# Optimization experiments

Hardware: AMD Instinct MI355X
Metric: run time of the kernel (lower is better)

## Reference

```python
import jax, jax.numpy as jnp
import numpy as np

B, N, S, D, ITERS = 128, 8192, 4, 32, 3
LN_EPS = 1e-5

def _ln(x, g, b):
    m = jnp.mean(x, axis=-1, keepdims=True)
    v = jnp.mean((x - m) ** 2, axis=-1, keepdims=True)
    return (x - m) * jax.lax.rsqrt(v + LN_EPS) * g + b

def setup_inputs() -> dict:
    key = jax.random.key(0)
    ks = jax.random.split(key, 16)
    s = 1.0 / np.sqrt(D)
    return {
        "x": jax.random.normal(ks[0], (B, N, D), jnp.float32),
        "slot_noise": jax.random.normal(ks[1], (B, S, D), jnp.float32),
        "slots_mu": jax.random.normal(ks[2], (1, 1, D), jnp.float32),
        "slots_logsigma": jnp.zeros((1, 1, D), jnp.float32),
        "Wq": jax.random.uniform(ks[3], (D, D), jnp.float32, -s, s),
        "Wk": jax.random.uniform(ks[4], (D, D), jnp.float32, -s, s),
        "Wv": jax.random.uniform(ks[5], (D, D), jnp.float32, -s, s),
        "gru_Wih": jax.random.uniform(ks[6], (3 * D, D), jnp.float32, -s, s),
        "gru_Whh": jax.random.uniform(ks[7], (3 * D, D), jnp.float32, -s, s),
        "gru_bih": jax.random.uniform(ks[8], (3 * D,), jnp.float32, -s, s),
        "gru_bhh": jax.random.uniform(ks[9], (3 * D,), jnp.float32, -s, s),
        "mlp_W1": jax.random.uniform(ks[10], (D, D), jnp.float32, -s, s),
        "mlp_b1": jax.random.uniform(ks[11], (D,), jnp.float32, -s, s),
        "mlp_W2": jax.random.uniform(ks[12], (D, D), jnp.float32, -s, s),
        "mlp_b2": jax.random.uniform(ks[13], (D,), jnp.float32, -s, s),
        "lnx_g": jnp.ones((D,), jnp.float32), "lnx_b": jnp.zeros((D,), jnp.float32),
        "lns_g": jnp.ones((D,), jnp.float32), "lns_b": jnp.zeros((D,), jnp.float32),
        "lnff_g": jnp.ones((D,), jnp.float32), "lnff_b": jnp.zeros((D,), jnp.float32),
    }

def reference(x, slot_noise, slots_mu, slots_logsigma, Wq, Wk, Wv,
              gru_Wih, gru_Whh, gru_bih, gru_bhh,
              mlp_W1, mlp_b1, mlp_W2, mlp_b2,
              lnx_g, lnx_b, lns_g, lns_b, lnff_g, lnff_b):
    d = x.shape[-1]
    scale = d ** (-0.5)
    xn = _ln(x, lnx_g, lnx_b)                      # [B,N,D]
    k = xn @ Wk.T                                  # [B,N,D] (x fixed -> hoist out of loop)
    v = xn @ Wv.T
    slots = slots_mu + slot_noise * jnp.exp(slots_logsigma)  # [B,S,D]
    for _ in range(ITERS):
        q = _ln(slots, lns_g, lns_b) @ Wq.T        # [B,S,D]
        attn = jnp.einsum('bsd,bnd->bsn', q, k) * scale
        attn = jax.nn.softmax(attn, axis=-1) + 1e-8
        attn = attn / jnp.sum(attn, axis=-1, keepdims=True)
        upd = jnp.einsum('bsn,bnd->bsd', attn, v)  # [B,S,D]
        # GRUCell (PyTorch gate order: r, z, n)
        gi = upd @ gru_Wih.T + gru_bih             # [B,S,3D]
        gh = slots @ gru_Whh.T + gru_bhh
        ir, iz, inn = jnp.split(gi, 3, axis=-1)
        hr, hz, hn = jnp.split(gh, 3, axis=-1)
        r = jax.nn.sigmoid(ir + hr)
        z = jax.nn.sigmoid(iz + hz)
        n = jnp.tanh(inn + r * hn)
        slots = (1.0 - z) * n + z * slots
        h = jax.nn.relu(_ln(slots, lnff_g, lnff_b) @ mlp_W1.T + mlp_b1)
        slots = slots + (h @ mlp_W2.T + mlp_b2)
    return slots.reshape(slots.shape[0], -1)
```

## Files before the change

### kernel.cpp

```cpp
#include <hip/hip_runtime.h>
#include <hip/hip_bf16.h>


#define Bn 128
#define Nn 8192
#define Sn 4
#define Dn 32
#define SCALE 0.17677669529663687f

#define Cn 16
#define RPB (Nn / Cn)
#define PT 256
#define RSTEP (PT / 4)
#define NSTEP (RPB / RSTEP)

#define WS_REQ ((size_t)(16384 + 16384 + Bn*Cn*Sn*Dn + Bn*Cn*Sn + Bn*Cn*Sn) * 4)

__device__ __forceinline__ float sigmoidf_(float v) { return 1.0f / (1.0f + __expf(-v)); }

__global__ __launch_bounds__(128)
void init_kernel(const float* __restrict__ noise, const float* __restrict__ mu,
                 const float* __restrict__ logsig,
                 const float* __restrict__ lns_g, const float* __restrict__ lns_b,
                 const float* __restrict__ Wq, const float* __restrict__ Wk,
                 float* __restrict__ slots, float* __restrict__ qt)
{
    const int b = blockIdx.x;
    const int tid = threadIdx.x;
    const int s = tid >> 5, d = tid & 31;
    __shared__ float sh_a[4][32];
    __shared__ float sh_b[4][32];

    float sv = mu[d] + noise[(b * Sn + s) * Dn + d] * __expf(logsig[d]);
    slots[(b * Sn + s) * Dn + d] = sv;

    float sx = sv, sxx = sv * sv;
    #pragma unroll
    for (int m = 1; m <= 16; m <<= 1) { sx += __shfl_xor(sx, m); sxx += __shfl_xor(sxx, m); }
    float mean = sx * (1.0f / 32.0f);
    float var  = sxx * (1.0f / 32.0f) - mean * mean;
    sh_a[s][d] = (sv - mean) * rsqrtf(var + 1e-5f) * lns_g[d] + lns_b[d];
    __syncthreads();

    float q = 0.0f;
    #pragma unroll 8
    for (int j = 0; j < 32; ++j) q = fmaf(Wq[d * 32 + j], sh_a[s][j], q);
    sh_b[s][d] = q;
    __syncthreads();

    float qtv = 0.0f;
    #pragma unroll 8
    for (int i = 0; i < 32; ++i) qtv = fmaf(sh_b[s][i], Wk[i * 32 + d], qtv);
    qt[(b * Sn + s) * Dn + d] = qtv * SCALE;
}

__global__ __launch_bounds__(PT)
void pass_kernel(const float* __restrict__ x, const float* __restrict__ qt,
                 const float* __restrict__ lnx_g, const float* __restrict__ lnx_b,
                 float* __restrict__ part_pa, float* __restrict__ part_pb,
                 float* __restrict__ part_ps)
{
    const int c = blockIdx.x;
    const int b = blockIdx.y;
    const int tid = threadIdx.x;
    const int sub = tid & 3, col0 = sub * 8;
    const int rg  = tid >> 2;

    float qg[4][8], qgs[4], qe[4];
    {
        const float* qtb = qt + (size_t)b * Sn * Dn;
        float g8[8], e8[8];
        #pragma unroll
        for (int k = 0; k < 8; ++k) { g8[k] = lnx_g[col0 + k]; e8[k] = lnx_b[col0 + k]; }
        #pragma unroll
        for (int s = 0; s < 4; ++s) {
            float sg = 0.f, se = 0.f;
            #pragma unroll
            for (int k = 0; k < 8; ++k) {
                float q = qtb[s * Dn + col0 + k];
                qg[s][k] = q * g8[k];
                sg += qg[s][k];
                se = fmaf(q, e8[k], se);
            }
            sg += __shfl_xor(sg, 1); sg += __shfl_xor(sg, 2);
            se += __shfl_xor(se, 1); se += __shfl_xor(se, 2);
            qgs[s] = sg; qe[s] = se;
        }
    }

    float pa[4][8], pb[4] = {0.f,0.f,0.f,0.f}, ps[4] = {0.f,0.f,0.f,0.f};
    #pragma unroll
    for (int s = 0; s < 4; ++s)
        #pragma unroll
        for (int k = 0; k < 8; ++k) pa[s][k] = 0.f;

    const float* xb = x + ((size_t)b * Nn + (size_t)c * RPB) * Dn;
    const float* p0 = xb + (size_t)rg * Dn + col0;
    float4 v0 = *(const float4*)(p0);
    float4 v1 = *(const float4*)(p0 + 4);

    for (int t = 0; t < NSTEP; ++t) {
        const int tn = (t + 1 < NSTEP) ? t + 1 : t;
        const float* pn = xb + (size_t)(tn * RSTEP + rg) * Dn + col0;
        float4 n0 = *(const float4*)(pn);
        float4 n1 = *(const float4*)(pn + 4);

        float xv[8] = {v0.x, v0.y, v0.z, v0.w, v1.x, v1.y, v1.z, v1.w};

        float sx = 0.f, sxx = 0.f, ds[4] = {0.f,0.f,0.f,0.f};
        #pragma unroll
        for (int k = 0; k < 8; ++k) {
            sx += xv[k];
            sxx = fmaf(xv[k], xv[k], sxx);
            #pragma unroll
            for (int s = 0; s < 4; ++s) ds[s] = fmaf(xv[k], qg[s][k], ds[s]);
        }
        sx += __shfl_xor(sx, 1); sxx += __shfl_xor(sxx, 1);
        #pragma unroll
        for (int s = 0; s < 4; ++s) ds[s] += __shfl_xor(ds[s], 1);
        sx += __shfl_xor(sx, 2); sxx += __shfl_xor(sxx, 2);
        #pragma unroll
        for (int s = 0; s < 4; ++s) ds[s] += __shfl_xor(ds[s], 2);

        float mean = sx * (1.0f / 32.0f);
        float var  = sxx * (1.0f / 32.0f) - mean * mean;
        float rs   = rsqrtf(var + 1e-5f);

        #pragma unroll
        for (int s = 0; s < 4; ++s) {
            float tt = fmaf(-mean, qgs[s], ds[s]);
            float lg = fmaf(rs, tt, qe[s]);
            float w  = __expf(lg);
            float al = w * rs;
            ps[s] += w;
            pb[s] = fmaf(al, mean, pb[s]);
            #pragma unroll
            for (int k = 0; k < 8; ++k) pa[s][k] = fmaf(al, xv[k], pa[s][k]);
        }
        v0 = n0; v1 = n1;
    }

    #pragma unroll
    for (int m = 4; m <= 32; m <<= 1) {
        #pragma unroll
        for (int s = 0; s < 4; ++s) {
            ps[s] += __shfl_xor(ps[s], m);
            pb[s] += __shfl_xor(pb[s], m);
            #pragma unroll
            for (int k = 0; k < 8; ++k) pa[s][k] += __shfl_xor(pa[s][k], m);
        }
    }

    __shared__ float ls_pa[4][4][32];
    __shared__ float ls_pb[4][4];
    __shared__ float ls_ps[4][4];
    const int wv = tid >> 6, lane = tid & 63;
    if (lane < 4) {
        #pragma unroll
        for (int s = 0; s < 4; ++s)
            #pragma unroll
            for (int k = 0; k < 8; ++k) ls_pa[wv][s][lane * 8 + k] = pa[s][k];
        if (lane == 0) {
            #pragma unroll
            for (int s = 0; s < 4; ++s) { ls_pb[wv][s] = pb[s]; ls_ps[wv][s] = ps[s]; }
        }
    }
    __syncthreads();
    if (tid < 128) {
        const int s = tid >> 5, d = tid & 31;
        float a = ls_pa[0][s][d] + ls_pa[1][s][d] + ls_pa[2][s][d] + ls_pa[3][s][d];
        part_pa[(((size_t)b * Cn + c) * Sn + s) * Dn + d] = a;
        if (d == 0) {
            part_pb[((size_t)b * Cn + c) * Sn + s] =
                ls_pb[0][s] + ls_pb[1][s] + ls_pb[2][s] + ls_pb[3][s];
            part_ps[((size_t)b * Cn + c) * Sn + s] =
                ls_ps[0][s] + ls_ps[1][s] + ls_ps[2][s] + ls_ps[3][s];
        }
    }
}

__global__ __launch_bounds__(128)
void update_kernel(const float* __restrict__ part_pa, const float* __restrict__ part_pb,
                   const float* __restrict__ part_ps,
                   const float* __restrict__ lnx_g, const float* __restrict__ lnx_b,
                   const float* __restrict__ Wv,
                   const float* __restrict__ Wih, const float* __restrict__ Whh,
                   const float* __restrict__ bih, const float* __restrict__ bhh,
                   const float* __restrict__ W1, const float* __restrict__ b1v,
                   const float* __restrict__ W2, const float* __restrict__ b2v,
                   const float* __restrict__ lns_g, const float* __restrict__ lns_b,
                   const float* __restrict__ lnff_g, const float* __restrict__ lnff_b,
                   const float* __restrict__ Wq, const float* __restrict__ Wk,
                   float* __restrict__ slots, float* __restrict__ qt,
                   float* __restrict__ out, int write_out, int write_qt)
{
    const int b = blockIdx.x;
    const int tid = threadIdx.x;
    const int s = tid >> 5, d = tid & 31;
    __shared__ float sh_a[4][32];
    __shared__ float sh_b[4][32];
    __shared__ float sh_sold[4][32];
    __shared__ float sh_h[4][32];

    float PA = 0.f, PB = 0.f, PS = 0.f;
    #pragma unroll
    for (int c = 0; c < Cn; ++c) {
        PA += part_pa[(((size_t)b * Cn + c) * Sn + s) * Dn + d];
        PB += part_pb[((size_t)b * Cn + c) * Sn + s];
        PS += part_ps[((size_t)b * Cn + c) * Sn + s];
    }
    float u = fmaf(lnx_g[d], PA - PB, PS * lnx_b[d]);
    const float renorm = 1.0f / (1.0f + (float)Nn * 1e-8f);
    sh_a[s][d] = (u / PS) * renorm;
    float sold = slots[(b * Sn + s) * Dn + d];
    sh_sold[s][d] = sold;
    __syncthreads();

    float upd = 0.f;
    #pragma unroll 8
    for (int j = 0; j < 32; ++j) upd = fmaf(Wv[d * 32 + j], sh_a[s][j], upd);
    sh_b[s][d] = upd;
    __syncthreads();

    float gi[3], gh[3];
    #pragma unroll
    for (int g3 = 0; g3 < 3; ++g3) {
        const int row = g3 * 32 + d;
        float a1 = bih[row], a2 = bhh[row];
        #pragma unroll 8
        for (int j = 0; j < 32; ++j) {
            a1 = fmaf(Wih[row * 32 + j], sh_b[s][j], a1);
            a2 = fmaf(Whh[row * 32 + j], sh_sold[s][j], a2);
        }
        gi[g3] = a1; gh[g3] = a2;
    }
    float r  = sigmoidf_(gi[0] + gh[0]);
    float z  = sigmoidf_(gi[1] + gh[1]);
    float nn = tanhf(gi[2] + r * gh[2]);
    float sv = (1.0f - z) * nn + z * sold;

    {
        float sx = sv, sxx = sv * sv;
        #pragma unroll
        for (int m = 1; m <= 16; m <<= 1) { sx += __shfl_xor(sx, m); sxx += __shfl_xor(sxx, m); }
        float mean = sx * (1.0f / 32.0f);
        float var  = sxx * (1.0f / 32.0f) - mean * mean;
        float rs   = rsqrtf(var + 1e-5f);
        __syncthreads();
        sh_a[s][d] = (sv - mean) * rs * lnff_g[d] + lnff_b[d];
    }
    __syncthreads();

    float h1 = b1v[d];
    #pragma unroll 8
    for (int j = 0; j < 32; ++j) h1 = fmaf(W1[d * 32 + j], sh_a[s][j], h1);
    sh_h[s][d] = fmaxf(h1, 0.0f);
    __syncthreads();

    float o = b2v[d];
    #pragma unroll 8
    for (int j = 0; j < 32; ++j) o = fmaf(W2[d * 32 + j], sh_h[s][j], o);
    float sfin = sv + o;

    slots[(b * Sn + s) * Dn + d] = sfin;
    if (write_out) out[(b * Sn + s) * Dn + d] = sfin;

    if (write_qt) {
        float sx = sfin, sxx = sfin * sfin;
        #pragma unroll
        for (int m = 1; m <= 16; m <<= 1) { sx += __shfl_xor(sx, m); sxx += __shfl_xor(sxx, m); }
        float mean = sx * (1.0f / 32.0f);
        float var  = sxx * (1.0f / 32.0f) - mean * mean;
        float rs   = rsqrtf(var + 1e-5f);
        __syncthreads();
        sh_a[s][d] = (sfin - mean) * rs * lns_g[d] + lns_b[d];
        __syncthreads();
        float q = 0.f;
        #pragma unroll 8
        for (int j = 0; j < 32; ++j) q = fmaf(Wq[d * 32 + j], sh_a[s][j], q);
        sh_b[s][d] = q;
        __syncthreads();
        float qtv = 0.f;
        #pragma unroll 8
        for (int i = 0; i < 32; ++i) qtv = fmaf(sh_b[s][i], Wk[i * 32 + d], qtv);
        qt[(b * Sn + s) * Dn + d] = qtv * SCALE;
    }
}

#define TPB 1024
#define NW (TPB / 64)
#define RPS (TPB / 4)
#define STEPS (Nn / RPS)

__global__ __launch_bounds__(TPB)
void slot_fused(const float* __restrict__ x, const float* __restrict__ noise,
                const float* __restrict__ mu, const float* __restrict__ logsig,
                const float* __restrict__ Wq, const float* __restrict__ Wk,
                const float* __restrict__ Wv,
                const float* __restrict__ Wih, const float* __restrict__ Whh,
                const float* __restrict__ bih, const float* __restrict__ bhh,
                const float* __restrict__ W1, const float* __restrict__ b1v,
                const float* __restrict__ W2, const float* __restrict__ b2v,
                const float* __restrict__ lnx_g, const float* __restrict__ lnx_b,
                const float* __restrict__ lns_g, const float* __restrict__ lns_b,
                const float* __restrict__ lnff_g, const float* __restrict__ lnff_b,
                float* __restrict__ out)
{
    const int b   = blockIdx.x;
    const int tid = threadIdx.x;
    __shared__ float slots_sh[Sn][Dn];
    __shared__ float qt_sh[Sn][Dn];
    __shared__ float a_sh[Sn][Dn];
    __shared__ float b_sh[Sn][Dn];
    __shared__ float h_sh[Sn][Dn];
    __shared__ float ls_u[NW][Sn][Dn];
    __shared__ float ls_s[NW][Sn];
    const int s128 = tid >> 5, d128 = tid & 31;

    if (tid < 128) {
        float sv = mu[d128] + noise[(b * Sn + s128) * Dn + d128] * __expf(logsig[d128]);
        slots_sh[s128][d128] = sv;
        float sx = sv, sxx = sv * sv;
        #pragma unroll
        for (int m = 1; m <= 16; m <<= 1) { sx += __shfl_xor(sx, m); sxx += __shfl_xor(sxx, m); }
        float mean = sx * (1.0f / 32.0f);
        float var  = sxx * (1.0f / 32.0f) - mean * mean;
        a_sh[s128][d128] = (sv - mean) * rsqrtf(var + 1e-5f) * lns_g[d128] + lns_b[d128];
    }
    __syncthreads();
    if (tid < 128) {
        float q = 0.f;
        #pragma unroll 8
        for (int j = 0; j < 32; ++j) q = fmaf(Wq[d128 * 32 + j], a_sh[s128][j], q);
        b_sh[s128][d128] = q;
    }
    __syncthreads();
    if (tid < 128) {
        float qv = 0.f;
        #pragma unroll 8
        for (int i = 0; i < 32; ++i) qv = fmaf(b_sh[s128][i], Wk[i * 32 + d128], qv);
        qt_sh[s128][d128] = qv * SCALE;
    }
    __syncthreads();

    const int sub = tid & 3, col0 = sub * 8;
    const int rg  = tid >> 2;
    float g_r[8], e_r[8];
    #pragma unroll
    for (int k = 0; k < 8; ++k) { g_r[k] = lnx_g[col0 + k]; e_r[k] = lnx_b[col0 + k]; }
    const float* xb = x + (size_t)b * Nn * Dn;
    float sv_reg = 0.f;

    for (int it = 0; it < 3; ++it) {
        float qt_r[4][8];
        #pragma unroll
        for (int s = 0; s < 4; ++s)
            #pragma unroll
            for (int k = 0; k < 8; ++k) qt_r[s][k] = qt_sh[s][col0 + k];
        float pu[4][8];
        float ps[4] = {0.f, 0.f, 0.f, 0.f};
        #pragma unroll
        for (int s = 0; s < 4; ++s)
            #pragma unroll
            for (int k = 0; k < 8; ++k) pu[s][k] = 0.f;

        const float* xr0 = xb + (size_t)rg * Dn + col0;
        float4 v0 = *(const float4*)(xr0);
        float4 v1 = *(const float4*)(xr0 + 4);
        #pragma unroll 2
        for (int t = 0; t < STEPS; ++t) {
            const float* xrn = xb + (size_t)((((t + 1) & (STEPS - 1)) * RPS) + rg) * Dn + col0;
            float4 n0 = *(const float4*)(xrn);
            float4 n1 = *(const float4*)(xrn + 4);
            float xv[8] = {v0.x, v0.y, v0.z, v0.w, v1.x, v1.y, v1.z, v1.w};
            float sx = 0.f, sxx = 0.f;
            #pragma unroll
            for (int k = 0; k < 8; ++k) { sx += xv[k]; sxx = fmaf(xv[k], xv[k], sxx); }
            sx += __shfl_xor(sx, 1); sxx += __shfl_xor(sxx, 1);
            sx += __shfl_xor(sx, 2); sxx += __shfl_xor(sxx, 2);
            float mean = sx * (1.0f / 32.0f);
            float var  = sxx * (1.0f / 32.0f) - mean * mean;
            float rs   = rsqrtf(var + 1e-5f);
            float xn[8];
            #pragma unroll
            for (int k = 0; k < 8; ++k) xn[k] = fmaf((xv[k] - mean) * rs, g_r[k], e_r[k]);
            #pragma unroll
            for (int s = 0; s < 4; ++s) {
                float a = 0.f;
                #pragma unroll
                for (int k = 0; k < 8; ++k) a = fmaf(xn[k], qt_r[s][k], a);
                a += __shfl_xor(a, 1);
                a += __shfl_xor(a, 2);
                float w = __expf(a);
                ps[s] += w;
                #pragma unroll
                for (int k = 0; k < 8; ++k) pu[s][k] = fmaf(w, xn[k], pu[s][k]);
            }
            v0 = n0; v1 = n1;
        }
        #pragma unroll
        for (int m = 4; m <= 32; m <<= 1) {
            #pragma unroll
            for (int s = 0; s < 4; ++s) {
                ps[s] += __shfl_xor(ps[s], m);
                #pragma unroll
                for (int k = 0; k < 8; ++k) pu[s][k] += __shfl_xor(pu[s][k], m);
            }
        }
        {
            const int wv = tid >> 6, lane = tid & 63;
            if (lane < 4) {
                #pragma unroll
                for (int s = 0; s < 4; ++s)
                    #pragma unroll
                    for (int k = 0; k < 8; ++k) ls_u[wv][s][lane * 8 + k] = pu[s][k];
                if (lane == 0) {
                    #pragma unroll
                    for (int s = 0; s < 4; ++s) ls_s[wv][s] = ps[s];
                }
            }
        }
        __syncthreads();
        if (tid < 128) {
            float u = 0.f, ss = 0.f;
            #pragma unroll
            for (int w = 0; w < NW; ++w) { u += ls_u[w][s128][d128]; ss += ls_s[w][s128]; }
            const float renorm = 1.0f / (1.0f + (float)Nn * 1e-8f);
            a_sh[s128][d128] = (u / ss) * renorm;
        }
        __syncthreads();
        if (tid < 128) {
            float upd = 0.f;
            #pragma unroll 8
            for (int j = 0; j < 32; ++j) upd = fmaf(Wv[d128 * 32 + j], a_sh[s128][j], upd);
            b_sh[s128][d128] = upd;
        }
        __syncthreads();
        if (tid < 128) {
            float gi[3], gh[3];
            #pragma unroll
            for (int g3 = 0; g3 < 3; ++g3) {
                const int row = g3 * 32 + d128;
                float a1 = bih[row], a2 = bhh[row];
                #pragma unroll 8
                for (int j = 0; j < 32; ++j) {
                    a1 = fmaf(Wih[row * 32 + j], b_sh[s128][j], a1);
                    a2 = fmaf(Whh[row * 32 + j], slots_sh[s128][j], a2);
                }
                gi[g3] = a1; gh[g3] = a2;
            }
            float r  = sigmoidf_(gi[0] + gh[0]);
            float z  = sigmoidf_(gi[1] + gh[1]);
            float nn = tanhf(gi[2] + r * gh[2]);
            sv_reg = (1.0f - z) * nn + z * slots_sh[s128][d128];
            float sx = sv_reg, sxx = sv_reg * sv_reg;
            #pragma unroll
            for (int m = 1; m <= 16; m <<= 1) { sx += __shfl_xor(sx, m); sxx += __shfl_xor(sxx, m); }
            float mean = sx * (1.0f / 32.0f);
            float var  = sxx * (1.0f / 32.0f) - mean * mean;
            a_sh[s128][d128] = (sv_reg - mean) * rsqrtf(var + 1e-5f) * lnff_g[d128] + lnff_b[d128];
        }
        __syncthreads();
        if (tid < 128) {
            float h = b1v[d128];
            #pragma unroll 8
            for (int j = 0; j < 32; ++j) h = fmaf(W1[d128 * 32 + j], a_sh[s128][j], h);
            h_sh[s128][d128] = fmaxf(h, 0.f);
        }
        __syncthreads();
        if (tid < 128) {
            float o = b2v[d128];
            #pragma unroll 8
            for (int j = 0; j < 32; ++j) o = fmaf(W2[d128 * 32 + j], h_sh[s128][j], o);
            float sfin = sv_reg + o;
            slots_sh[s128][d128] = sfin;
            if (it < 2) {
                float sx = sfin, sxx = sfin * sfin;
                #pragma unroll
                for (int m = 1; m <= 16; m <<= 1) { sx += __shfl_xor(sx, m); sxx += __shfl_xor(sxx, m); }
                float mean = sx * (1.0f / 32.0f);
                float var  = sxx * (1.0f / 32.0f) - mean * mean;
                a_sh[s128][d128] = (sfin - mean) * rsqrtf(var + 1e-5f) * lns_g[d128] + lns_b[d128];
            }
        }
        __syncthreads();
        if (it < 2) {
            if (tid < 128) {
                float q = 0.f;
                #pragma unroll 8
                for (int j = 0; j < 32; ++j) q = fmaf(Wq[d128 * 32 + j], a_sh[s128][j], q);
                b_sh[s128][d128] = q;
            }
            __syncthreads();
            if (tid < 128) {
                float qv = 0.f;
                #pragma unroll 8
                for (int i = 0; i < 32; ++i) qv = fmaf(b_sh[s128][i], Wk[i * 32 + d128], qv);
                qt_sh[s128][d128] = qv * SCALE;
            }
            __syncthreads();
        }
    }
    if (tid < 128)
        out[(size_t)b * 128 + tid] = slots_sh[s128][d128];
}

extern "C" void kernel_launch(void* const* d_in, const int* in_sizes, int n_in,
                              void* d_out, int out_size, void* d_ws, size_t ws_size,
                              hipStream_t stream)
{
    const float* x      = (const float*)d_in[0];
    const float* noise  = (const float*)d_in[1];
    const float* mu     = (const float*)d_in[2];
    const float* logsig = (const float*)d_in[3];
    const float* Wq     = (const float*)d_in[4];
    const float* Wk     = (const float*)d_in[5];
    const float* Wv     = (const float*)d_in[6];
    const float* Wih    = (const float*)d_in[7];
    const float* Whh    = (const float*)d_in[8];
    const float* bih    = (const float*)d_in[9];
    const float* bhh    = (const float*)d_in[10];
    const float* W1     = (const float*)d_in[11];
    const float* b1v    = (const float*)d_in[12];
    const float* W2     = (const float*)d_in[13];
    const float* b2v    = (const float*)d_in[14];
    const float* lnx_g  = (const float*)d_in[15];
    const float* lnx_b  = (const float*)d_in[16];
    const float* lns_g  = (const float*)d_in[17];
    const float* lns_b  = (const float*)d_in[18];
    const float* lnff_g = (const float*)d_in[19];
    const float* lnff_b = (const float*)d_in[20];
    float* out = (float*)d_out;

    if (ws_size >= WS_REQ) {
        float* ws      = (float*)d_ws;
        float* slots   = ws;
        float* qt      = ws + 16384;
        float* part_pa = ws + 32768;
        float* part_pb = ws + 32768 + Bn * Cn * Sn * Dn;
        float* part_ps = part_pb + Bn * Cn * Sn;

        init_kernel<<<Bn, 128, 0, stream>>>(noise, mu, logsig, lns_g, lns_b, Wq, Wk,
                                            slots, qt);
        for (int it = 0; it < 3; ++it) {
            pass_kernel<<<dim3(Cn, Bn), PT, 0, stream>>>(x, qt, lnx_g, lnx_b,
                                                         part_pa, part_pb, part_ps);
            update_kernel<<<Bn, 128, 0, stream>>>(part_pa, part_pb, part_ps,
                                                  lnx_g, lnx_b, Wv, Wih, Whh, bih, bhh,
                                                  W1, b1v, W2, b2v, lns_g, lns_b,
                                                  lnff_g, lnff_b, Wq, Wk, slots, qt, out,
                                                  (it == 2) ? 1 : 0, (it < 2) ? 1 : 0);
        }
    } else {
        slot_fused<<<Bn, TPB, 0, stream>>>(x, noise, mu, logsig, Wq, Wk, Wv,
                                           Wih, Whh, bih, bhh, W1, b1v, W2, b2v,
                                           lnx_g, lnx_b, lns_g, lns_b, lnff_g, lnff_b,
                                           out);
    }
}
```

Baseline: 134.6 us.

## Cache normalized x as bf16 and fuse slot update into attention passes

The first pass computes LayerNorm of x once and stores it as a bf16 buffer. Later passes read this half-size buffer and skip the per-row LayerNorm math. The small per-batch slot update (GRU, MLP, query projection) is recomputed redundantly at the start of each pass block, removing separate init and update launches. This trades bf16 rounding error in the keys and values for less memory traffic and fewer kernel launches.

Result: slower. 173.3 us (+28.7%).

```diff
diff --git a/kernel.cpp b/kernel.cpp
--- a/kernel.cpp
+++ b/kernel.cpp
@@ -7,6 +7,7 @@
 #define Sn 4
 #define Dn 32
 #define SCALE 0.17677669529663687f
+#define RENORM (1.0f / (1.0f + (float)Nn * 1e-8f))
 
 #define Cn 16
 #define RPB (Nn / Cn)
@@ -14,130 +15,286 @@
 #define RSTEP (PT / 4)
 #define NSTEP (RPB / RSTEP)
 
-#define WS_REQ ((size_t)(16384 + 16384 + Bn*Cn*Sn*Dn + Bn*Cn*Sn + Bn*Cn*Sn) * 4)
+#define WS_REQ ((size_t)(3 * Bn * Sn * Dn + 3 * Bn * Cn * Sn * Dn + 3 * Bn * Cn * Sn) * 4 \
+                + (size_t)Bn * Nn * Dn * 2)
 
 __device__ __forceinline__ float sigmoidf_(float v) { return 1.0f / (1.0f + __expf(-v)); }
-
-__global__ __launch_bounds__(128)
-void init_kernel(const float* __restrict__ noise, const float* __restrict__ mu,
-                 const float* __restrict__ logsig,
-                 const float* __restrict__ lns_g, const float* __restrict__ lns_b,
-                 const float* __restrict__ Wq, const float* __restrict__ Wk,
-                 float* __restrict__ slots, float* __restrict__ qt)
+__device__ __forceinline__ unsigned f2bf_rne(float f) {
+    unsigned u = __float_as_uint(f);
+    u += 0x7fffu + ((u >> 16) & 1u);
+    return u >> 16;
+}
+__device__ __forceinline__ float bflo2f(unsigned u) { return __uint_as_float(u << 16); }
+__device__ __forceinline__ float bfhi2f(unsigned u) { return __uint_as_float(u & 0xffff0000u); }
+
+template<int KIND, int WANT_QT>
+__device__ __forceinline__ void chain_fn(
+    int b, int tid,
+    const float* __restrict__ pa_prev, const float* __restrict__ ps_prev,
+    const float* __restrict__ slots_prev,
+    const float* __restrict__ noise, const float* __restrict__ mu,
+    const float* __restrict__ logsig,
+    const float* __restrict__ Wv,
+    const float* __restrict__ Wih, const float* __restrict__ Whh,
+    const float* __restrict__ bih, const float* __restrict__ bhh,
+    const float* __restrict__ W1, const float* __restrict__ b1v,
+    const float* __restrict__ W2, const float* __restrict__ b2v,
+    const float* __restrict__ lns_g, const float* __restrict__ lns_b,
+    const float* __restrict__ lnff_g, const float* __restrict__ lnff_b,
+    const float* __restrict__ Wq, const float* __restrict__ Wk,
+    float (*qt_sh)[Dn], float (*ta)[Dn], float (*tb)[Dn],
+    float* __restrict__ store)
 {
-    const int b = blockIdx.x;
-    const int tid = threadIdx.x;
-    const int s = tid >> 5, d = tid & 31;
-    __shared__ float sh_a[4][32];
-    __shared__ float sh_b[4][32];
-
-    float sv = mu[d] + noise[(b * Sn + s) * Dn + d] * __expf(logsig[d]);
-    slots[(b * Sn + s) * Dn + d] = sv;
-
-    float sx = sv, sxx = sv * sv;
+    const int s = (tid >> 5) & 3, d = tid & 31;
+    const bool act = tid < 128;
+    float sfin = 0.f;
+
+    if constexpr (KIND == 0) {
+        if (act)
+            sfin = mu[d] + noise[(b * Sn + s) * Dn + d] * __expf(logsig[d]);
+    } else {
+        float sv_c = 0.f, lnffv = 0.f;
+        if (act) {
+            float u = 0.f, PS = 0.f;
+            #pragma unroll
+            for (int c = 0; c < Cn; ++c) {
+                u  += pa_prev[(((size_t)b * Cn + c) * Sn + s) * Dn + d];
+                PS += ps_prev[((size_t)b * Cn + c) * Sn + s];
+            }
+            ta[s][d] = (u / PS) * RENORM;
+            tb[s][d] = slots_prev[(b * Sn + s) * Dn + d];
+        }
+        __syncthreads();
+        float updv = 0.f;
+        if (act) {
+            #pragma unroll 8
+            for (int j = 0; j < 32; ++j) updv = fmaf(Wv[d * 32 + j], ta[s][j], updv);
+        }
+        __syncthreads();
+        if (act) ta[s][d] = updv;
+        __syncthreads();
+        if (act) {
+            float gi[3], gh[3];
+            #pragma unroll
+            for (int g3 = 0; g3 < 3; ++g3) {
+                const int row = g3 * 32 + d;
+                float a1 = bih[row], a2 = bhh[row];
+                #pragma unroll 8
+                for (int j = 0; j < 32; ++j) {
+                    a1 = fmaf(Wih[row * 32 + j], ta[s][j], a1);
+                    a2 = fmaf(Whh[row * 32 + j], tb[s][j], a2);
+                }
+                gi[g3] = a1; gh[g3] = a2;
+            }
+            float r  = sigmoidf_(gi[0] + gh[0]);
+            float z  = sigmoidf_(gi[1] + gh[1]);
+            float nn = tanhf(gi[2] + r * gh[2]);
+            sv_c = (1.0f - z) * nn + z * tb[s][d];
+            float sx = sv_c, sxx = sv_c * sv_c;
+            #pragma unroll
+            for (int m = 1; m <= 16; m <<= 1) { sx += __shfl_xor(sx, m); sxx += __shfl_xor(sxx, m); }
+            float mean = sx * (1.0f / 32.0f);
+            float var  = sxx * (1.0f / 32.0f) - mean * mean;
+            lnffv = (sv_c - mean) * rsqrtf(var + 1e-5f) * lnff_g[d] + lnff_b[d];
+        }
+        __syncthreads();
+        if (act) ta[s][d] = lnffv;
+        __syncthreads();
+        if (act) {
+            float h = b1v[d];
+            #pragma unroll 8
+            for (int j = 0; j < 32; ++j) h = fmaf(W1[d * 32 + j], ta[s][j], h);
+            tb[s][d] = fmaxf(h, 0.f);
+        }
+        __syncthreads();
+        if (act) {
+            float o = b2v[d];
+            #pragma unroll 8
+            for (int j = 0; j < 32; ++j) o = fmaf(W2[d * 32 + j], tb[s][j], o);
+            sfin = sv_c + o;
+        }
+    }
+
+    if (act && store) store[(b * Sn + s) * Dn + d] = sfin;
+
+    if constexpr (WANT_QT) {
+        float lnsv = 0.f;
+        if (act) {
+            float sx = sfin, sxx = sfin * sfin;
+            #pragma unroll
+            for (int m = 1; m <= 16; m <<= 1) { sx += __shfl_xor(sx, m); sxx += __shfl_xor(sxx, m); }
+            float mean = sx * (1.0f / 32.0f);
+            float var  = sxx * (1.0f / 32.0f) - mean * mean;
+            lnsv = (sfin - mean) * rsqrtf(var + 1e-5f) * lns_g[d] + lns_b[d];
+        }
+        __syncthreads();
+        if (act) ta[s][d] = lnsv;
+        __syncthreads();
+        if (act) {
+            float q = 0.f;
+            #pragma unroll 8
+            for (int j = 0; j < 32; ++j) q = fmaf(Wq[d * 32 + j], ta[s][j], q);
+            tb[s][d] = q;
+        }
+        __syncthreads();
+        if (act) {
+            float qv = 0.f;
+            #pragma unroll 8
+            for (int i = 0; i < 32; ++i) qv = fmaf(tb[s][i], Wk[i * 32 + d], qv);
+            qt_sh[s][d] = qv * SCALE;
+        }
+        __syncthreads();
+    }
+}
+
+template<int IT>
+__global__ __launch_bounds__(PT)
+void pass_k(const float* __restrict__ x, unsigned short* __restrict__ y,
+            const float* __restrict__ noise, const float* __restrict__ mu,
+            const float* __restrict__ logsig,
+            const float* __restrict__ Wq, const float* __restrict__ Wk,
+            const float* __restrict__ Wv,
+            const float* __restrict__ Wih, const float* __restrict__ Whh,
+            const float* __restrict__ bih, const float* __restrict__ bhh,
+            const float* __restrict__ W1, const float* __restrict__ b1v,
+            const float* __restrict__ W2, const float* __restrict__ b2v,
+            const float* __restrict__ lnx_g, const float* __restrict__ lnx_b,
+            const float* __restrict__ lns_g, const float* __restrict__ lns_b,
+            const float* __restrict__ lnff_g, const float* __restrict__ lnff_b,
+            const float* __restrict__ slots_prev, float* __restrict__ slots_cur,
+            const float* __restrict__ pa_prev, const float* __restrict__ ps_prev,
+            float* __restrict__ pa_cur, float* __restrict__ ps_cur)
+{
+    const int c = blockIdx.x, b = blockIdx.y, tid = threadIdx.x;
+    __shared__ float qt_sh[Sn][Dn], ta[Sn][Dn], tb[Sn][Dn];
+    __shared__ float ls_pa[4][Sn][Dn];
+    __shared__ float ls_ps[4][Sn];
+
+    chain_fn<(IT == 0 ? 0 : 1), 1>(b, tid, pa_prev, ps_prev, slots_prev,
+        noise, mu, logsig, Wv, Wih, Whh, bih, bhh, W1, b1v, W2, b2v,
+        lns_g, lns_b, lnff_g, lnff_b, Wq, Wk,
+        qt_sh, ta, tb, (c == 0) ? slots_cur : nullptr);
+
+    const int sub = tid & 3, col0 = sub * 8, rg = tid >> 2;
+    float pa[4][8];
+    float ps[4] = {0.f, 0.f, 0.f, 0.f};
     #pragma unroll
-    for (int m = 1; m <= 16; m <<= 1) { sx += __shfl_xor(sx, m); sxx += __shfl_xor(sxx, m); }
-    float mean = sx * (1.0f / 32.0f);
-    float var  = sxx * (1.0f / 32.0f) - mean * mean;
-    sh_a[s][d] = (sv - mean) * rsqrtf(var + 1e-5f) * lns_g[d] + lns_b[d];
-    __syncthreads();
-
-    float q = 0.0f;
-    #pragma unroll 8
-    for (int j = 0; j < 32; ++j) q = fmaf(Wq[d * 32 + j], sh_a[s][j], q);
-    sh_b[s][d] = q;
-    __syncthreads();
-
-    float qtv = 0.0f;
-    #pragma unroll 8
-    for (int i = 0; i < 32; ++i) qtv = fmaf(sh_b[s][i], Wk[i * 32 + d], qtv);
-    qt[(b * Sn + s) * Dn + d] = qtv * SCALE;
-}
-
-__global__ __launch_bounds__(PT)
-void pass_kernel(const float* __restrict__ x, const float* __restrict__ qt,
-                 const float* __restrict__ lnx_g, const float* __restrict__ lnx_b,
-                 float* __restrict__ part_pa, float* __restrict__ part_pb,
-                 float* __restrict__ part_ps)
-{
-    const int c = blockIdx.x;
-    const int b = blockIdx.y;
-    const int tid = threadIdx.x;
-    const int sub = tid & 3, col0 = sub * 8;
-    const int rg  = tid >> 2;
-
-    float qg[4][8], qgs[4], qe[4];
-    {
-        const float* qtb = qt + (size_t)b * Sn * Dn;
-        float g8[8], e8[8];
-        #pragma unroll
-        for (int k = 0; k < 8; ++k) { g8[k] = lnx_g[col0 + k]; e8[k] = lnx_b[col0 + k]; }
+    for (int s = 0; s < 4; ++s)
+        #pragma unroll
+        for (int k = 0; k < 8; ++k) pa[s][k] = 0.f;
+
+    if constexpr (IT == 0) {
+        float g_r[8], e_r[8];
+        #pragma unroll
+        for (int k = 0; k < 8; ++k) { g_r[k] = lnx_g[col0 + k]; e_r[k] = lnx_b[col0 + k]; }
+        float qg[4][8], qgs[4], qe[4];
         #pragma unroll
         for (int s = 0; s < 4; ++s) {
             float sg = 0.f, se = 0.f;
             #pragma unroll
             for (int k = 0; k < 8; ++k) {
-                float q = qtb[s * Dn + col0 + k];
-                qg[s][k] = q * g8[k];
+                float q = qt_sh[s][col0 + k];
+                qg[s][k] = q * g_r[k];
                 sg += qg[s][k];
-                se = fmaf(q, e8[k], se);
+                se = fmaf(q, e_r[k], se);
             }
             sg += __shfl_xor(sg, 1); sg += __shfl_xor(sg, 2);
             se += __shfl_xor(se, 1); se += __shfl_xor(se, 2);
             qgs[s] = sg; qe[s] = se;
         }
-    }
-
-    float pa[4][8], pb[4] = {0.f,0.f,0.f,0.f}, ps[4] = {0.f,0.f,0.f,0.f};
-    #pragma unroll
-    for (int s = 0; s < 4; ++s)
-        #pragma unroll
-        for (int k = 0; k < 8; ++k) pa[s][k] = 0.f;
-
-    const float* xb = x + ((size_t)b * Nn + (size_t)c * RPB) * Dn;
-    const float* p0 = xb + (size_t)rg * Dn + col0;
-    float4 v0 = *(const float4*)(p0);
-    float4 v1 = *(const float4*)(p0 + 4);
-
-    for (int t = 0; t < NSTEP; ++t) {
-        const int tn = (t + 1 < NSTEP) ? t + 1 : t;
-        const float* pn = xb + (size_t)(tn * RSTEP + rg) * Dn + col0;
-        float4 n0 = *(const float4*)(pn);
-        float4 n1 = *(const float4*)(pn + 4);
-
-        float xv[8] = {v0.x, v0.y, v0.z, v0.w, v1.x, v1.y, v1.z, v1.w};
-
-        float sx = 0.f, sxx = 0.f, ds[4] = {0.f,0.f,0.f,0.f};
-        #pragma unroll
-        for (int k = 0; k < 8; ++k) {
-            sx += xv[k];
-            sxx = fmaf(xv[k], xv[k], sxx);
-            #pragma unroll
-            for (int s = 0; s < 4; ++s) ds[s] = fmaf(xv[k], qg[s][k], ds[s]);
-        }
-        sx += __shfl_xor(sx, 1); sxx += __shfl_xor(sxx, 1);
-        #pragma unroll
-        for (int s = 0; s < 4; ++s) ds[s] += __shfl_xor(ds[s], 1);
-        sx += __shfl_xor(sx, 2); sxx += __shfl_xor(sxx, 2);
-        #pragma unroll
-        for (int s = 0; s < 4; ++s) ds[s] += __shfl_xor(ds[s], 2);
-
-        float mean = sx * (1.0f / 32.0f);
-        float var  = sxx * (1.0f / 32.0f) - mean * mean;
-        float rs   = rsqrtf(var + 1e-5f);
-
-        #pragma unroll
-        for (int s = 0; s < 4; ++s) {
-            float tt = fmaf(-mean, qgs[s], ds[s]);
-            float lg = fmaf(rs, tt, qe[s]);
-            float w  = __expf(lg);
-            float al = w * rs;
-            ps[s] += w;
-            pb[s] = fmaf(al, mean, pb[s]);
-            #pragma unroll
-            for (int k = 0; k < 8; ++k) pa[s][k] = fmaf(al, xv[k], pa[s][k]);
-        }
-        v0 = n0; v1 = n1;
+
+        const float* xb = x + ((size_t)b * Nn + (size_t)c * RPB) * Dn;
+        unsigned short* yb = y + ((size_t)b * Nn + (size_t)c * RPB) * Dn;
+        const float* p0 = xb + (size_t)rg * Dn + col0;
+        float4 v0 = *(const float4*)(p0);
+        float4 v1 = *(const float4*)(p0 + 4);
+
+        for (int t = 0; t < NSTEP; ++t) {
+            const int tn = (t + 1 < NSTEP) ? t + 1 : t;
+            const float* pn = xb + (size_t)(tn * RSTEP + rg) * Dn + col0;
+            float4 n0 = *(const float4*)(pn);
+            float4 n1 = *(const float4*)(pn + 4);
+
+            float xv[8] = {v0.x, v0.y, v0.z, v0.w, v1.x, v1.y, v1.z, v1.w};
+            float sx = 0.f, sxx = 0.f, ds[4] = {0.f, 0.f, 0.f, 0.f};
+            #pragma unroll
+            for (int k = 0; k < 8; ++k) {
+                sx += xv[k];
+                sxx = fmaf(xv[k], xv[k], sxx);
+                #pragma unroll
+                for (int s = 0; s < 4; ++s) ds[s] = fmaf(xv[k], qg[s][k], ds[s]);
+            }
+            sx += __shfl_xor(sx, 1); sxx += __shfl_xor(sxx, 1);
+            #pragma unroll
+            for (int s = 0; s < 4; ++s) ds[s] += __shfl_xor(ds[s], 1);
+            sx += __shfl_xor(sx, 2); sxx += __shfl_xor(sxx, 2);
+            #pragma unroll
+            for (int s = 0; s < 4; ++s) ds[s] += __shfl_xor(ds[s], 2);
+
+            float mean = sx * (1.0f / 32.0f);
+            float var  = sxx * (1.0f / 32.0f) - mean * mean;
+            float rs   = rsqrtf(var + 1e-5f);
+
+            float xn[8];
+            #pragma unroll
+            for (int k = 0; k < 8; ++k) xn[k] = fmaf((xv[k] - mean) * rs, g_r[k], e_r[k]);
+
+            uint4 yw;
+            yw.x = (f2bf_rne(xn[1]) << 16) | f2bf_rne(xn[0]);
+            yw.y = (f2bf_rne(xn[3]) << 16) | f2bf_rne(xn[2]);
+            yw.z = (f2bf_rne(xn[5]) << 16) | f2bf_rne(xn[4]);
+            yw.w = (f2bf_rne(xn[7]) << 16) | f2bf_rne(xn[6]);
+            *(uint4*)(yb + (size_t)(t * RSTEP + rg) * Dn + col0) = yw;
+
+            #pragma unroll
+            for (int s = 0; s < 4; ++s) {
+                float lg = fmaf(rs, fmaf(-mean, qgs[s], ds[s]), qe[s]);
+                float w  = __expf(lg);
+                ps[s] += w;
+                #pragma unroll
+                for (int k = 0; k < 8; ++k) pa[s][k] = fmaf(w, xn[k], pa[s][k]);
+            }
+            v0 = n0; v1 = n1;
+        }
+    } else {
+        float qt_r[4][8];
+        #pragma unroll
+        for (int s = 0; s < 4; ++s)
+            #pragma unroll
+            for (int k = 0; k < 8; ++k) qt_r[s][k] = qt_sh[s][col0 + k];
+
+        const unsigned short* yb = y + ((size_t)b * Nn + (size_t)c * RPB) * Dn;
+        uint4 cv = *(const uint4*)(yb + (size_t)rg * Dn + col0);
+
+        for (int t = 0; t < NSTEP; ++t) {
+            const int tn = (t + 1 < NSTEP) ? t + 1 : t;
+            uint4 nv = *(const uint4*)(yb + (size_t)(tn * RSTEP + rg) * Dn + col0);
+
+            float yv[8];
+            yv[0] = bflo2f(cv.x); yv[1] = bfhi2f(cv.x);
+            yv[2] = bflo2f(cv.y); yv[3] = bfhi2f(cv.y);
+            yv[4] = bflo2f(cv.z); yv[5] = bfhi2f(cv.z);
+            yv[6] = bflo2f(cv.w); yv[7] = bfhi2f(cv.w);
+
+            float ds[4] = {0.f, 0.f, 0.f, 0.f};
+            #pragma unroll
+            for (int k = 0; k < 8; ++k)
+                #pragma unroll
+                for (int s = 0; s < 4; ++s) ds[s] = fmaf(yv[k], qt_r[s][k], ds[s]);
+            #pragma unroll
+            for (int s = 0; s < 4; ++s) ds[s] += __shfl_xor(ds[s], 1);
+            #pragma unroll
+            for (int s = 0; s < 4; ++s) ds[s] += __shfl_xor(ds[s], 2);
+
+            #pragma unroll
+            for (int s = 0; s < 4; ++s) {
+                float w = __expf(ds[s]);
+                ps[s] += w;
+                #pragma unroll
+                for (int k = 0; k < 8; ++k) pa[s][k] = fmaf(w, yv[k], pa[s][k]);
+            }
+            cv = nv;
+        }
     }
 
     #pragma unroll
@@ -145,15 +302,10 @@
         #pragma unroll
         for (int s = 0; s < 4; ++s) {
             ps[s] += __shfl_xor(ps[s], m);
-            pb[s] += __shfl_xor(pb[s], m);
             #pragma unroll
             for (int k = 0; k < 8; ++k) pa[s][k] += __shfl_xor(pa[s][k], m);
         }
     }
-
-    __shared__ float ls_pa[4][4][32];
-    __shared__ float ls_pb[4][4];
-    __shared__ float ls_ps[4][4];
     const int wv = tid >> 6, lane = tid & 63;
     if (lane < 4) {
         #pragma unroll
@@ -162,129 +314,38 @@
             for (int k = 0; k < 8; ++k) ls_pa[wv][s][lane * 8 + k] = pa[s][k];
         if (lane == 0) {
             #pragma unroll
-            for (int s = 0; s < 4; ++s) { ls_pb[wv][s] = pb[s]; ls_ps[wv][s] = ps[s]; }
+            for (int s = 0; s < 4; ++s) ls_ps[wv][s] = ps[s];
         }
     }
     __syncthreads();
     if (tid < 128) {
         const int s = tid >> 5, d = tid & 31;
         float a = ls_pa[0][s][d] + ls_pa[1][s][d] + ls_pa[2][s][d] + ls_pa[3][s][d];
-        part_pa[(((size_t)b * Cn + c) * Sn + s) * Dn + d] = a;
-        if (d == 0) {
-            part_pb[((size_t)b * Cn + c) * Sn + s] =
-                ls_pb[0][s] + ls_pb[1][s] + ls_pb[2][s] + ls_pb[3][s];
-            part_ps[((size_t)b * Cn + c) * Sn + s] =
+        pa_cur[(((size_t)b * Cn + c) * Sn + s) * Dn + d] = a;
+        if (d == 0)
+            ps_cur[((size_t)b * Cn + c) * Sn + s] =
                 ls_ps[0][s] + ls_ps[1][s] + ls_ps[2][s] + ls_ps[3][s];
-        }
     }
 }
 
 __global__ __launch_bounds__(128)
-void update_kernel(const float* __restrict__ part_pa, const float* __restrict__ part_pb,
-                   const float* __restrict__ part_ps,
-                   const float* __restrict__ lnx_g, const float* __restrict__ lnx_b,
-                   const float* __restrict__ Wv,
-                   const float* __restrict__ Wih, const float* __restrict__ Whh,
-                   const float* __restrict__ bih, const float* __restrict__ bhh,
-                   const float* __restrict__ W1, const float* __restrict__ b1v,
-                   const float* __restrict__ W2, const float* __restrict__ b2v,
-                   const float* __restrict__ lns_g, const float* __restrict__ lns_b,
-                   const float* __restrict__ lnff_g, const float* __restrict__ lnff_b,
-                   const float* __restrict__ Wq, const float* __restrict__ Wk,
-                   float* __restrict__ slots, float* __restrict__ qt,
-                   float* __restrict__ out, int write_out, int write_qt)
+void final_k(const float* __restrict__ Wv,
+             const float* __restrict__ Wih, const float* __restrict__ Whh,
+             const float* __restrict__ bih, const float* __restrict__ bhh,
+             const float* __restrict__ W1, const float* __restrict__ b1v,
+             const float* __restrict__ W2, const float* __restrict__ b2v,
+             const float* __restrict__ lns_g, const float* __restrict__ lns_b,
+             const float* __restrict__ lnff_g, const float* __restrict__ lnff_b,
+             const float* __restrict__ Wq, const float* __restrict__ Wk,
+             const float* __restrict__ slots_prev,
+             const float* __restrict__ pa_prev, const float* __restrict__ ps_prev,
+             float* __restrict__ out)
 {
-    const int b = blockIdx.x;
-    const int tid = threadIdx.x;
-    const int s = tid >> 5, d = tid & 31;
-    __shared__ float sh_a[4][32];
-    __shared__ float sh_b[4][32];
-    __shared__ float sh_sold[4][32];
-    __shared__ float sh_h[4][32];
-
-    float PA = 0.f, PB = 0.f, PS = 0.f;
-    #pragma unroll
-    for (int c = 0; c < Cn; ++c) {
-        PA += part_pa[(((size_t)b * Cn + c) * Sn + s) * Dn + d];
-        PB += part_pb[((size_t)b * Cn + c) * Sn + s];
-        PS += part_ps[((size_t)b * Cn + c) * Sn + s];
-    }
-    float u = fmaf(lnx_g[d], PA - PB, PS * lnx_b[d]);
-    const float renorm = 1.0f / (1.0f + (float)Nn * 1e-8f);
-    sh_a[s][d] = (u / PS) * renorm;
-    float sold = slots[(b * Sn + s) * Dn + d];
-    sh_sold[s][d] = sold;
-    __syncthreads();
-
-    float upd = 0.f;
-    #pragma unroll 8
-    for (int j = 0; j < 32; ++j) upd = fmaf(Wv[d * 32 + j], sh_a[s][j], upd);
-    sh_b[s][d] = upd;
-    __syncthreads();
-
-    float gi[3], gh[3];
-    #pragma unroll
-    for (int g3 = 0; g3 < 3; ++g3) {
-        const int row = g3 * 32 + d;
-        float a1 = bih[row], a2 = bhh[row];
-        #pragma unroll 8
-        for (int j = 0; j < 32; ++j) {
-            a1 = fmaf(Wih[row * 32 + j], sh_b[s][j], a1);
-            a2 = fmaf(Whh[row * 32 + j], sh_sold[s][j], a2);
-        }
-        gi[g3] = a1; gh[g3] = a2;
-    }
-    float r  = sigmoidf_(gi[0] + gh[0]);
-    float z  = sigmoidf_(gi[1] + gh[1]);
-    float nn = tanhf(gi[2] + r * gh[2]);
-    float sv = (1.0f - z) * nn + z * sold;
-
-    {
-        float sx = sv, sxx = sv * sv;
-        #pragma unroll
-        for (int m = 1; m <= 16; m <<= 1) { sx += __shfl_xor(sx, m); sxx += __shfl_xor(sxx, m); }
-        float mean = sx * (1.0f / 32.0f);
-        float var  = sxx * (1.0f / 32.0f) - mean * mean;
-        float rs   = rsqrtf(var + 1e-5f);
-        __syncthreads();
-        sh_a[s][d] = (sv - mean) * rs * lnff_g[d] + lnff_b[d];
-    }
-    __syncthreads();
-
-    float h1 = b1v[d];
-    #pragma unroll 8
-    for (int j = 0; j < 32; ++j) h1 = fmaf(W1[d * 32 + j], sh_a[s][j], h1);
-    sh_h[s][d] = fmaxf(h1, 0.0f);
-    __syncthreads();
-
-    float o = b2v[d];
-    #pragma unroll 8
-    for (int j = 0; j < 32; ++j) o = fmaf(W2[d * 32 + j], sh_h[s][j], o);
-    float sfin = sv + o;
-
-    slots[(b * Sn + s) * Dn + d] = sfin;
-    if (write_out) out[(b * Sn + s) * Dn + d] = sfin;
-
-    if (write_qt) {
-        float sx = sfin, sxx = sfin * sfin;
-        #pragma unroll
-        for (int m = 1; m <= 16; m <<= 1) { sx += __shfl_xor(sx, m); sxx += __shfl_xor(sxx, m); }
-        float mean = sx * (1.0f / 32.0f);
-        float var  = sxx * (1.0f / 32.0f) - mean * mean;
-        float rs   = rsqrtf(var + 1e-5f);
-        __syncthreads();
-        sh_a[s][d] = (sfin - mean) * rs * lns_g[d] + lns_b[d];
-        __syncthreads();
-        float q = 0.f;
-        #pragma unroll 8
-        for (int j = 0; j < 32; ++j) q = fmaf(Wq[d * 32 + j], sh_a[s][j], q);
-        sh_b[s][d] = q;
-        __syncthreads();
-        float qtv = 0.f;
-        #pragma unroll 8
-        for (int i = 0; i < 32; ++i) qtv = fmaf(sh_b[s][i], Wk[i * 32 + d], qtv);
-        qt[(b * Sn + s) * Dn + d] = qtv * SCALE;
-    }
+    const int b = blockIdx.x, tid = threadIdx.x;
+    __shared__ float qt_sh[Sn][Dn], ta[Sn][Dn], tb[Sn][Dn];
+    chain_fn<1, 0>(b, tid, pa_prev, ps_prev, slots_prev,
+        nullptr, nullptr, nullptr, Wv, Wih, Whh, bih, bhh, W1, b1v, W2, b2v,
+        lns_g, lns_b, lnff_g, lnff_b, Wq, Wk, qt_sh, ta, tb, out);
 }
 
 #define TPB 1024
@@ -425,8 +486,7 @@
             float u = 0.f, ss = 0.f;
             #pragma unroll
             for (int w = 0; w < NW; ++w) { u += ls_u[w][s128][d128]; ss += ls_s[w][s128]; }
-            const float renorm = 1.0f / (1.0f + (float)Nn * 1e-8f);
-            a_sh[s128][d128] = (u / ss) * renorm;
+            a_sh[s128][d128] = (u / ss) * RENORM;
         }
         __syncthreads();
         if (tid < 128) {
@@ -533,24 +593,32 @@
     float* out = (float*)d_out;
 
     if (ws_size >= WS_REQ) {
-        float* ws      = (float*)d_ws;
-        float* slots   = ws;
-        float* qt      = ws + 16384;
-        float* part_pa = ws + 32768;
-        float* part_pb = ws + 32768 + Bn * Cn * Sn * Dn;
-        float* part_ps = part_pb + Bn * Cn * Sn;
-
-        init_kernel<<<Bn, 128, 0, stream>>>(noise, mu, logsig, lns_g, lns_b, Wq, Wk,
-                                            slots, qt);
-        for (int it = 0; it < 3; ++it) {
-            pass_kernel<<<dim3(Cn, Bn), PT, 0, stream>>>(x, qt, lnx_g, lnx_b,
-                                                         part_pa, part_pb, part_ps);
-            update_kernel<<<Bn, 128, 0, stream>>>(part_pa, part_pb, part_ps,
-                                                  lnx_g, lnx_b, Wv, Wih, Whh, bih, bhh,
-                                                  W1, b1v, W2, b2v, lns_g, lns_b,
-                                                  lnff_g, lnff_b, Wq, Wk, slots, qt, out,
-                                                  (it == 2) ? 1 : 0, (it < 2) ? 1 : 0);
-        }
+        float* wsf    = (float*)d_ws;
+        float* slots0 = wsf;
+        float* slots1 = slots0 + Bn * Sn * Dn;
+        float* slots2 = slots1 + Bn * Sn * Dn;
+        float* pa0    = slots2 + Bn * Sn * Dn;
+        float* pa1    = pa0 + Bn * Cn * Sn * Dn;
+        float* pa2    = pa1 + Bn * Cn * Sn * Dn;
+        float* ps0    = pa2 + Bn * Cn * Sn * Dn;
+        float* ps1    = ps0 + Bn * Cn * Sn;
+        float* ps2    = ps1 + Bn * Cn * Sn;
+        unsigned short* ybuf = (unsigned short*)(ps2 + Bn * Cn * Sn);
+
+        pass_k<0><<<dim3(Cn, Bn), PT, 0, stream>>>(x, ybuf, noise, mu, logsig,
+            Wq, Wk, Wv, Wih, Whh, bih, bhh, W1, b1v, W2, b2v,
+            lnx_g, lnx_b, lns_g, lns_b, lnff_g, lnff_b,
+            nullptr, slots0, nullptr, nullptr, pa0, ps0);
+        pass_k<1><<<dim3(Cn, Bn), PT, 0, stream>>>(x, ybuf, noise, mu, logsig,
+            Wq, Wk, Wv, Wih, Whh, bih, bhh, W1, b1v, W2, b2v,
+            lnx_g, lnx_b, lns_g, lns_b, lnff_g, lnff_b,
+            slots0, slots1, pa0, ps0, pa1, ps1);
+        pass_k<2><<<dim3(Cn, Bn), PT, 0, stream>>>(x, ybuf, noise, mu, logsig,
+            Wq, Wk, Wv, Wih, Whh, bih, bhh, W1, b1v, W2, b2v,
+            lnx_g, lnx_b, lns_g, lns_b, lnff_g, lnff_b,
+            slots1, slots2, pa1, ps1, pa2, ps2);
+        final_k<<<Bn, 128, 0, stream>>>(Wv, Wih, Whh, bih, bhh, W1, b1v, W2, b2v,
+            lns_g, lns_b, lnff_g, lnff_b, Wq, Wk, slots2, pa2, ps2, out);
     } else {
         slot_fused<<<Bn, TPB, 0, stream>>>(x, noise, mu, logsig, Wq, Wk, Wv,
                                            Wih, Whh, bih, bhh, W1, b1v, W2, b2v,
```
